# Optimization experiments

Measured on AMD Instinct MI355X. Metric: run time of the kernel, lower is better.

Reference implementation:

```python
import jax, jax.numpy as jnp
import numpy as np

TEMPERATURE = 0.1
NUM_CLASSES = 100


def setup_inputs() -> dict:
    key = jax.random.key(0)
    k1, k2 = jax.random.split(key)
    embeddings = jax.random.normal(k1, (8192, 128), dtype=jnp.float32)
    labels = jax.random.randint(k2, (8192,), 0, NUM_CLASSES, dtype=jnp.int64)
    return {"embeddings": embeddings, "labels": labels}


def reference(embeddings, labels):
    # L2-normalize rows (eps matches torch.nn.functional.normalize clamp)
    norm = jnp.maximum(jnp.linalg.norm(embeddings, axis=1, keepdims=True), 1e-12)
    e = embeddings / norm
    sim = jnp.matmul(e, e.T) / TEMPERATURE  # [N, N]
    n = sim.shape[0]
    eye = jnp.eye(n, dtype=bool)
    # positives: same label, excluding self
    pos = (labels[None, :] == labels[:, None]) & ~eye
    # The per-row torch loop computes soft-target cross-entropy over all
    # non-diagonal entries: row_loss_i = -sum_{j in pos(i)} log_softmax(sim[i, j!=i])_j.
    # log_softmax is permutation-invariant, so concatenation order is irrelevant.
    neg_inf = jnp.finfo(sim.dtype).min
    masked = jnp.where(eye, neg_inf, sim)
    logz = jax.nn.logsumexp(masked, axis=1, keepdims=True)  # [N, 1]
    logp = sim - logz  # [N, N]
    row_loss = -jnp.sum(jnp.where(pos, logp, 0.0), axis=1)  # rows with no positives contribute 0
    return jnp.sum(row_loss) / n
```

## Files before the change

kernel.cpp:

```cpp
#include <hip/hip_runtime.h>


#define N 8192
#define D 128
#define NCLS 100
#define NTILE 512
#define RLCAP 256
#define MWIN 8
#define YGRID 32
#define XGRID 36
#define LDS_TILES 20
#define K2E 14.4269504088896340736f
#define LN2 0.69314718055994530942f

typedef __bf16 bf16x8 __attribute__((ext_vector_type(8)));
typedef float f32x4 __attribute__((ext_vector_type(4)));

#define EBF_OFF  0x000000u
#define ENORM_OFF 0x200000u
#define CNT_OFF  0x600000u
#define Z_OFF    0x600200u
#define RL_OFF   0x608200u
#define S_OFF    0x621200u
#define ZERO_SZ  (512u + 32768u)

__device__ __forceinline__ unsigned short f32_to_bf16_rne(float f) {
    unsigned int u = __float_as_uint(f);
    u += 0x7fffu + ((u >> 16) & 1u);
    return (unsigned short)(u >> 16);
}


__global__ __launch_bounds__(256) void prep_kernel(
        const float* __restrict__ emb, const int* __restrict__ labels,
        unsigned char* __restrict__ ebf, int* __restrict__ cnt,
        float* __restrict__ enorm, int* __restrict__ rowlist) {
    const int w    = threadIdx.x >> 6;
    const int lane = threadIdx.x & 63;
    const int h    = lane >> 5;
    const int li   = lane & 31;
    const int row  = blockIdx.x * 8 + w * 2 + h;

    const float4 v = *(const float4*)(emb + (size_t)row * D + li * 4);
    float ss = v.x * v.x + v.y * v.y + v.z * v.z + v.w * v.w;
    #pragma unroll
    for (int off = 16; off; off >>= 1) ss += __shfl_xor(ss, off);
    const float inv = 1.0f / fmaxf(sqrtf(ss), 1e-12f);
    const float e0 = v.x * inv, e1 = v.y * inv, e2 = v.z * inv, e3 = v.w * inv;

    const int grp = row >> 4, col = row & 15;
    const int c = li >> 3, q = (li >> 1) & 3, jh = li & 1;
    uint2 packed;
    packed.x = (unsigned)f32_to_bf16_rne(e0) | ((unsigned)f32_to_bf16_rne(e1) << 16);
    packed.y = (unsigned)f32_to_bf16_rne(e2) | ((unsigned)f32_to_bf16_rne(e3) << 16);
    *(uint2*)(ebf + grp * 4096 + c * 1024 + q * 256 + col * 16 + jh * 8) = packed;

    *(float4*)(enorm + (size_t)row * D + li * 4) = make_float4(e0, e1, e2, e3);

    if (li == 0) {
        const int lab = labels[row];
        int slot = atomicAdd(&cnt[lab], 1);
        slot = slot < RLCAP ? slot : RLCAP - 1;
        rowlist[lab * RLCAP + slot] = row;
    }
}

__global__ __launch_bounds__(256) void zsum_kernel(
        const unsigned char* __restrict__ ebf, float* __restrict__ z,
        const float* __restrict__ enorm, const int* __restrict__ cnt,
        const int* __restrict__ rowlist, float* __restrict__ S) {
    const int t = threadIdx.x;

    if (blockIdx.x >= 32) {
        const int eidx = (blockIdx.x - 32) * YGRID + blockIdx.y;
        if (eidx >= NCLS || t >= 128) return;
        const int d = t;
        const int n = cnt[eidx] < RLCAP ? cnt[eidx] : RLCAP;
        const int* rl = rowlist + eidx * RLCAP;
        float acc = 0.0f;
        int idx = 0;
        for (; idx + 4 <= n; idx += 4) {
            const int r0 = rl[idx], r1 = rl[idx + 1], r2 = rl[idx + 2], r3 = rl[idx + 3];
            acc += enorm[(size_t)r0 * D + d] + enorm[(size_t)r1 * D + d]
                 + enorm[(size_t)r2 * D + d] + enorm[(size_t)r3 * D + d];
        }
        for (; idx < n; ++idx)
            acc += enorm[(size_t)rl[idx] * D + d];
        S[eidx * D + d] = acc;
        return;
    }

    __shared__ float zcol[LDS_TILES * 16];
    const int w    = t >> 6;
    const int lane = t & 63;
    const int q    = lane >> 4;
    const int col  = lane & 15;
    const int bi   = blockIdx.x;
    const int y    = blockIdx.y;
    const int ti0  = bi * 16 + w * 4;
    const int m_lo = y * MWIN + 1;
    const bool lowhalf = (bi < 16);

    for (int e = t; e < LDS_TILES * 16; e += 256) zcol[e] = 0.0f;

    bf16x8 a[4][4];
    #pragma unroll
    for (int g = 0; g < 4; ++g) {
        const unsigned char* ag = ebf + (size_t)(ti0 + g) * 4096 + lane * 16;
        #pragma unroll
        for (int c = 0; c < 4; ++c) a[g][c] = *(const bf16x8*)(ag + c * 1024);
    }

    float zacc[4][4] = {{0.f,0.f,0.f,0.f},{0.f,0.f,0.f,0.f},
                        {0.f,0.f,0.f,0.f},{0.f,0.f,0.f,0.f}};

    __syncthreads();

    if (y == 0) {
        #pragma unroll
        for (int g = 0; g < 4; ++g) {
            const unsigned char* bg = ebf + (size_t)(ti0 + g) * 4096 + lane * 16;
            bf16x8 bd[4];
            #pragma unroll
            for (int c = 0; c < 4; ++c) bd[c] = *(const bf16x8*)(bg + c * 1024);
            f32x4 acc = {0.f, 0.f, 0.f, 0.f};
            #pragma unroll
            for (int c = 0; c < 4; ++c)
                acc = __builtin_amdgcn_mfma_f32_16x16x32_bf16(a[g][c], bd[c], acc, 0, 0, 0);
            #pragma unroll
            for (int r = 0; r < 4; ++r)
                zacc[g][r] += (col == q * 4 + r) ? 0.0f
                    : __builtin_amdgcn_exp2f(fmaf(acc[r], K2E, -K2E));
        }
    }

    const int ns = MWIN + ((y == 29 || y == 30 || (y == 31 && lowhalf)) ? 1 : 0);
    const int m_x = 228 + y;

    bf16x8 bc[4];
    {
        const int tj = (ti0 + m_lo) & (NTILE - 1);
        const unsigned char* bg = ebf + (size_t)tj * 4096 + lane * 16;
        #pragma unroll
        for (int c = 0; c < 4; ++c) bc[c] = *(const bf16x8*)(bg + c * 1024);
    }

    #pragma unroll 2
    for (int s = 0; s < ns; ++s) {
        const int m = (s < MWIN) ? (m_lo + s) : m_x;

        const int sn = (s + 1 < ns) ? s + 1 : s;
        const int mn = (sn < MWIN) ? (m_lo + sn) : m_x;
        bf16x8 bn[4];
        {
            const int tjn = (ti0 + mn) & (NTILE - 1);
            const unsigned char* bg = ebf + (size_t)tjn * 4096 + lane * 16;
            #pragma unroll
            for (int c = 0; c < 4; ++c) bn[c] = *(const bf16x8*)(bg + c * 1024);
        }

        float ctot = 0.0f;
        #pragma unroll
        for (int g = 0; g < 4; ++g) {
            const int d = m - g;
            const bool act = (d >= 1 && d <= 255) || (d == 256 && lowhalf);
            if (act) {
                f32x4 acc = {0.f, 0.f, 0.f, 0.f};
                __builtin_amdgcn_s_setprio(1);
                #pragma unroll
                for (int c = 0; c < 4; ++c)
                    acc = __builtin_amdgcn_mfma_f32_16x16x32_bf16(a[g][c], bc[c], acc, 0, 0, 0);
                __builtin_amdgcn_s_setprio(0);
                #pragma unroll
                for (int r = 0; r < 4; ++r) {
                    const float p = __builtin_amdgcn_exp2f(fmaf(acc[r], K2E, -K2E));
                    zacc[g][r] += p;
                    ctot += p;
                }
            }
        }

        ctot += __shfl_xor(ctot, 16);
        ctot += __shfl_xor(ctot, 32);
        if (q == 0 && ctot != 0.0f) {
            if (s < MWIN) {
                const int rel = w * 4 + (m - m_lo);
                atomicAdd(&zcol[rel * 16 + col], ctot);
            } else {
                const int tj = (ti0 + m) & (NTILE - 1);
                atomicAdd(&z[tj * 16 + col], ctot);
            }
        }

        #pragma unroll
        for (int c = 0; c < 4; ++c) bc[c] = bn[c];
    }

    #pragma unroll
    for (int g = 0; g < 4; ++g)
        #pragma unroll
        for (int r = 0; r < 4; ++r) {
            float zv = zacc[g][r];
            zv += __shfl_xor(zv, 1);
            zv += __shfl_xor(zv, 2);
            zv += __shfl_xor(zv, 4);
            zv += __shfl_xor(zv, 8);
            if (col == 0)
                atomicAdd(&z[(ti0 + g) * 16 + q * 4 + r], zv);
        }

    __syncthreads();
    for (int e = t; e < LDS_TILES * 16; e += 256) {
        const float v = zcol[e];
        if (v != 0.0f) {
            const int tj = (bi * 16 + m_lo + (e >> 4)) & (NTILE - 1);
            atomicAdd(&z[tj * 16 + (e & 15)], v);
        }
    }
}

__global__ __launch_bounds__(1024) void final_kernel(
        const int* __restrict__ labels, const int* __restrict__ cnt,
        const float* __restrict__ z, const float* __restrict__ S,
        float* __restrict__ out) {
    __shared__ float part[16];
    const int tid = threadIdx.x;
    float acc = 0.0f;
    #pragma unroll
    for (int k = 0; k < N / 1024; ++k) {
        const int row = k * 1024 + tid;
        const int P = cnt[labels[row]] - 1;
        if (P > 0)
            acc += (float)P * fmaf(LN2, __builtin_amdgcn_logf(z[row]), 10.0f);
    }
    #pragma unroll
    for (int k = 0; k < (NCLS * D + 1023) / 1024; ++k) {
        const int idx = k * 1024 + tid;
        if (idx < NCLS * D) {
            const float sv = S[idx];
            acc -= 10.0f * sv * sv;
        }
    }
    #pragma unroll
    for (int off = 32; off; off >>= 1) acc += __shfl_xor(acc, off);
    if ((tid & 63) == 0) part[tid >> 6] = acc;
    __syncthreads();
    if (tid == 0) {
        float tot = 0.0f;
        #pragma unroll
        for (int w = 0; w < 16; ++w) tot += part[w];
        out[0] = (tot + 10.0f * (float)N) * (1.0f / (float)N);
    }
}

extern "C" void kernel_launch(void* const* d_in, const int* in_sizes, int n_in,
                              void* d_out, int out_size, void* d_ws, size_t ws_size,
                              hipStream_t stream) {
    const float* emb  = (const float*)d_in[0];
    const int* labels = (const int*)d_in[1];
    float* out        = (float*)d_out;
    char* ws          = (char*)d_ws;

    unsigned char* ebf = (unsigned char*)(ws + EBF_OFF);
    float* enorm       = (float*)(ws + ENORM_OFF);
    int*   cnt         = (int*)(ws + CNT_OFF);
    float* z           = (float*)(ws + Z_OFF);
    int*   rowlist     = (int*)(ws + RL_OFF);
    float* S           = (float*)(ws + S_OFF);

    hipMemsetAsync(ws + CNT_OFF, 0, ZERO_SZ, stream);

    prep_kernel<<<N / 8, 256, 0, stream>>>(emb, labels, ebf, cnt, enorm, rowlist);
    zsum_kernel<<<dim3(XGRID, YGRID), 256, 0, stream>>>(ebf, z, enorm, cnt, rowlist, S);
    final_kernel<<<1, 1024, 0, stream>>>(labels, cnt, z, S, out);
}
```

Baseline: 115.9 us.

## Fold temperature/log2e scale into bf16 embeddings, rotate tile order per wave

Pre-scales the bf16 embeddings by sqrt(log2e/T), so the MFMA output is already in log2 units and exp2 can be applied directly. This drops the per-element FMA and the max-shift of -K2E, which removes the offset that previously kept exp2 arguments near zero. Also rotates each wave's tile visit order to spread LDS atomic contention and vectorizes the accumulators. The risk is that without the shift, exp values reach up to about e^10 and lose the stabilization; bf16 rounding of the scaled values also changes.

```diff
diff --git a/kernel.cpp b/kernel.cpp
--- a/kernel.cpp
+++ b/kernel.cpp
@@ -10,7 +10,7 @@
 #define YGRID 32
 #define XGRID 36
 #define LDS_TILES 20
-#define K2E 14.4269504088896340736f
+#define SQK 3.79828256f
 #define LN2 0.69314718055994530942f
 
 typedef __bf16 bf16x8 __attribute__((ext_vector_type(8)));
@@ -51,8 +51,8 @@
     const int grp = row >> 4, col = row & 15;
     const int c = li >> 3, q = (li >> 1) & 3, jh = li & 1;
     uint2 packed;
-    packed.x = (unsigned)f32_to_bf16_rne(e0) | ((unsigned)f32_to_bf16_rne(e1) << 16);
-    packed.y = (unsigned)f32_to_bf16_rne(e2) | ((unsigned)f32_to_bf16_rne(e3) << 16);
+    packed.x = (unsigned)f32_to_bf16_rne(e0 * SQK) | ((unsigned)f32_to_bf16_rne(e1 * SQK) << 16);
+    packed.y = (unsigned)f32_to_bf16_rne(e2 * SQK) | ((unsigned)f32_to_bf16_rne(e3 * SQK) << 16);
     *(uint2*)(ebf + grp * 4096 + c * 1024 + q * 256 + col * 16 + jh * 8) = packed;
 
     *(float4*)(enorm + (size_t)row * D + li * 4) = make_float4(e0, e1, e2, e3);
@@ -111,8 +111,8 @@
         for (int c = 0; c < 4; ++c) a[g][c] = *(const bf16x8*)(ag + c * 1024);
     }
 
-    float zacc[4][4] = {{0.f,0.f,0.f,0.f},{0.f,0.f,0.f,0.f},
-                        {0.f,0.f,0.f,0.f},{0.f,0.f,0.f,0.f}};
+    f32x4 zacc4[4] = {{0.f,0.f,0.f,0.f},{0.f,0.f,0.f,0.f},
+                      {0.f,0.f,0.f,0.f},{0.f,0.f,0.f,0.f}};
 
     __syncthreads();
 
@@ -129,17 +129,20 @@
                 acc = __builtin_amdgcn_mfma_f32_16x16x32_bf16(a[g][c], bd[c], acc, 0, 0, 0);
             #pragma unroll
             for (int r = 0; r < 4; ++r)
-                zacc[g][r] += (col == q * 4 + r) ? 0.0f
-                    : __builtin_amdgcn_exp2f(fmaf(acc[r], K2E, -K2E));
+                zacc4[g][r] += (col == q * 4 + r) ? 0.0f
+                    : __builtin_amdgcn_exp2f(acc[r]);
         }
     }
 
     const int ns = MWIN + ((y == 29 || y == 30 || (y == 31 && lowhalf)) ? 1 : 0);
     const int m_x = 228 + y;
 
+    const int rot = 2 * w;
+
     bf16x8 bc[4];
     {
-        const int tj = (ti0 + m_lo) & (NTILE - 1);
+        const int m0 = m_lo + (rot & (MWIN - 1));
+        const int tj = (ti0 + m0) & (NTILE - 1);
         const unsigned char* bg = ebf + (size_t)tj * 4096 + lane * 16;
         #pragma unroll
         for (int c = 0; c < 4; ++c) bc[c] = *(const bf16x8*)(bg + c * 1024);
@@ -147,10 +150,10 @@
 
     #pragma unroll 2
     for (int s = 0; s < ns; ++s) {
-        const int m = (s < MWIN) ? (m_lo + s) : m_x;
+        const int m = (s < MWIN) ? (m_lo + ((s + rot) & (MWIN - 1))) : m_x;
 
         const int sn = (s + 1 < ns) ? s + 1 : s;
-        const int mn = (sn < MWIN) ? (m_lo + sn) : m_x;
+        const int mn = (sn < MWIN) ? (m_lo + ((sn + rot) & (MWIN - 1))) : m_x;
         bf16x8 bn[4];
         {
             const int tjn = (ti0 + mn) & (NTILE - 1);
@@ -159,7 +162,7 @@
             for (int c = 0; c < 4; ++c) bn[c] = *(const bf16x8*)(bg + c * 1024);
         }
 
-        float ctot = 0.0f;
+        f32x4 ct = {0.f, 0.f, 0.f, 0.f};
         #pragma unroll
         for (int g = 0; g < 4; ++g) {
             const int d = m - g;
@@ -171,15 +174,16 @@
                 for (int c = 0; c < 4; ++c)
                     acc = __builtin_amdgcn_mfma_f32_16x16x32_bf16(a[g][c], bc[c], acc, 0, 0, 0);
                 __builtin_amdgcn_s_setprio(0);
+                f32x4 p;
                 #pragma unroll
-                for (int r = 0; r < 4; ++r) {
-                    const float p = __builtin_amdgcn_exp2f(fmaf(acc[r], K2E, -K2E));
-                    zacc[g][r] += p;
-                    ctot += p;
-                }
+                for (int r = 0; r < 4; ++r)
+                    p[r] = __builtin_amdgcn_exp2f(acc[r]);
+                zacc4[g] += p;
+                ct += p;
             }
         }
 
+        float ctot = (ct[0] + ct[1]) + (ct[2] + ct[3]);
         ctot += __shfl_xor(ctot, 16);
         ctot += __shfl_xor(ctot, 32);
         if (q == 0 && ctot != 0.0f) {
@@ -200,7 +204,7 @@
     for (int g = 0; g < 4; ++g)
         #pragma unroll
         for (int r = 0; r < 4; ++r) {
-            float zv = zacc[g][r];
+            float zv = zacc4[g][r];
             zv += __shfl_xor(zv, 1);
             zv += __shfl_xor(zv, 2);
             zv += __shfl_xor(zv, 4);
@@ -231,7 +235,7 @@
         const int row = k * 1024 + tid;
         const int P = cnt[labels[row]] - 1;
         if (P > 0)
-            acc += (float)P * fmaf(LN2, __builtin_amdgcn_logf(z[row]), 10.0f);
+            acc += (float)P * (LN2 * __builtin_amdgcn_logf(z[row]));
     }
     #pragma unroll
     for (int k = 0; k < (NCLS * D + 1023) / 1024; ++k) {
```

Result: slower. 125.1 us (+7.9%).
